# Performance work log

Measured on AMD Instinct MI355X. Metric: run time of the kernel, lower is better.

Reference implementation:

```python
import jax, jax.numpy as jnp
import numpy as np

B, N, C, H = 4, 1024, 1024, 16
DH = C // H  # 64
EPS = 1e-5   # nn.LayerNorm default


def _layernorm(x, g, b):
    m = x.mean(-1, keepdims=True)
    v = ((x - m) ** 2).mean(-1, keepdims=True)
    return (x - m) * jax.lax.rsqrt(v + EPS) * g + b


def _rot_half(x):
    d = x.shape[-1] // 2
    return jnp.concatenate([-x[..., d:], x[..., :d]], axis=-1)


def _apply_rope_cat(x, emb):
    # emb: [N, 2*DH] = sin || cos (torch tensor_split(2, -1) order)
    sin, cos = jnp.split(emb, 2, axis=-1)  # each [N, DH]
    return x * cos + _rot_half(x) * sin


def setup_inputs() -> dict:
    key = jax.random.key(0)
    ks = jax.random.split(key, 12)
    s = 0.02
    x = jax.random.normal(ks[0], (B, N, C), jnp.float32)
    delta_t_emb = jax.random.normal(ks[1], (B, N, C), jnp.float32)
    v_residual_v1 = jax.random.normal(ks[2], (B, H, N, DH), jnp.float32)
    # realistic rope table: sin||cos, each DH wide (freqs repeated twice for rotate_half)
    pos = jnp.arange(N, dtype=jnp.float32)
    inv_freq = 1.0 / (10000.0 ** (jnp.arange(0, DH // 2, dtype=jnp.float32) / (DH // 2)))
    freqs = pos[:, None] * inv_freq[None, :]          # [N, DH/2]
    freqs = jnp.concatenate([freqs, freqs], axis=-1)  # [N, DH]
    rope = jnp.concatenate([jnp.sin(freqs), jnp.cos(freqs)], axis=-1)  # [N, 2*DH]
    Wqkv = jax.random.normal(ks[3], (3 * C, C), jnp.float32) * s
    bqkv = jnp.zeros((3 * C,), jnp.float32)
    Wdt = jax.random.normal(ks[4], (3 * C, C), jnp.float32) * s
    bdt = jnp.zeros((3 * C,), jnp.float32)
    qn_g = jnp.ones((DH,), jnp.float32); qn_b = jnp.zeros((DH,), jnp.float32)
    kn_g = jnp.ones((DH,), jnp.float32); kn_b = jnp.zeros((DH,), jnp.float32)
    lamb1 = jnp.asarray(0.5, jnp.float32)
    lamb2 = jnp.asarray(0.5, jnp.float32)
    Wproj = jax.random.normal(ks[5], (C, C), jnp.float32) * s
    bproj = jnp.zeros((C,), jnp.float32)
    return {
        "x": x, "rope": rope, "delta_t_emb": delta_t_emb, "v_residual_v1": v_residual_v1,
        "Wqkv": Wqkv, "bqkv": bqkv, "Wdt": Wdt, "bdt": bdt,
        "qn_g": qn_g, "qn_b": qn_b, "kn_g": kn_g, "kn_b": kn_b,
        "lamb1": lamb1, "lamb2": lamb2, "Wproj": Wproj, "bproj": bproj,
    }


def reference(x, rope, delta_t_emb, v_residual_v1, Wqkv, bqkv, Wdt, bdt,
              qn_g, qn_b, kn_g, kn_b, lamb1, lamb2, Wproj, bproj):
    b, n, c = x.shape
    # fused QKV: [B,N,3C] -> [3,B,H,N,DH]
    qkv = (jnp.einsum('bnc,oc->bno', x, Wqkv) + bqkv).reshape(b, n, 3, H, DH)
    qkv = jnp.transpose(qkv, (2, 0, 3, 1, 4))
    q, k, v = qkv[0], qkv[1], qkv[2]
    # delta-t additive embeddings
    dqkv = (jnp.einsum('bnc,oc->bno', delta_t_emb, Wdt) + bdt).reshape(b, n, 3, H, DH)
    dqkv = jnp.transpose(dqkv, (2, 0, 3, 1, 4))
    q = q + dqkv[0]; k = k + dqkv[1]; v = v + dqkv[2]
    # value-residual mixing
    v = lamb1 * v + lamb2 * v_residual_v1
    # qk layernorm over head_dim
    q = _layernorm(q, qn_g, qn_b)
    k = _layernorm(k, kn_g, kn_b)
    # RoPE (num_prefix_tokens = 0, rotate_half=True)
    q = _apply_rope_cat(q, rope)
    k = _apply_rope_cat(k, rope)
    # SDPA, non-causal, no dropout
    scale = 1.0 / jnp.sqrt(jnp.asarray(DH, x.dtype))
    scores = jnp.einsum('bhqd,bhkd->bhqk', q, k) * scale
    attn = jax.nn.softmax(scores, axis=-1)
    out = jnp.einsum('bhqk,bhkd->bhqd', attn, v)
    # [B,H,N,DH] -> [B,N,C], output norm is Identity (scale_norm=False)
    out = jnp.transpose(out, (0, 2, 1, 3)).reshape(b, n, c)
    out = jnp.einsum('bnc,oc->bno', out, Wproj) + bproj
    return out
```

## Files before the change

kernel.cpp:

```cpp
#include <hip/hip_runtime.h>
#include <stdint.h>

typedef unsigned short u16;
typedef __attribute__((ext_vector_type(8))) short short8;
typedef __attribute__((ext_vector_type(4))) float f32x4;
typedef __attribute__((ext_vector_type(4))) unsigned short u16x4;
typedef __attribute__((ext_vector_type(4))) unsigned int u32x4;

#define DEVI __device__ __forceinline__

DEVI u16 f2bf(float f) {
  uint32_t u = __builtin_bit_cast(uint32_t, f);
  u += 0x7fffu + ((u >> 16) & 1u);
  return (u16)(u >> 16);
}

DEVI float bf2f(u16 u) {
  uint32_t v = ((uint32_t)u) << 16;
  return __builtin_bit_cast(float, v);
}

DEVI uint32_t cvt_pk_bf16(float lo, float hi) {
  uint32_t r;
  asm("v_cvt_pk_bf16_f32 %0, %1, %2" : "=v"(r) : "v"(lo), "v"(hi));
  return r;
}

DEVI void gload_lds16(const void* g, void* l) {
  __builtin_amdgcn_global_load_lds(
      (const __attribute__((address_space(1))) void*)g,
      (__attribute__((address_space(3))) void*)(uint32_t)(uintptr_t)l,
      16, 0, 0);
}

__global__ void cvt_all(const float* __restrict__ x, const float* __restrict__ dte,
                        const float* __restrict__ Wqkv, const float* __restrict__ Wdt,
                        const float* __restrict__ Wproj,
                        u16* __restrict__ A_cat, u16* __restrict__ W_cat,
                        u16* __restrict__ Wp) {
  const long T0 = (long)4096 * 2048 / 4;
  const long T1 = (long)3072 * 2048 / 4;
  const long T2 = (long)1024 * 1024 / 4;
  for (long v = (long)blockIdx.x * 256 + threadIdx.x; v < T0 + T1 + T2;
       v += (long)gridDim.x * 256) {
    const float* src;
    u16* dst;
    if (v < T0) {
      const long i = v * 4;
      const long row = i >> 11, c = i & 2047;
      src = (c < 1024) ? (x + row * 1024 + c) : (dte + row * 1024 + (c - 1024));
      dst = A_cat + i;
    } else if (v < T0 + T1) {
      const long i = (v - T0) * 4;
      const long row = i >> 11, c = i & 2047;
      src = (c < 1024) ? (Wqkv + row * 1024 + c) : (Wdt + row * 1024 + (c - 1024));
      dst = W_cat + i;
    } else {
      const long i = (v - T0 - T1) * 4;
      src = Wproj + i;
      dst = Wp + i;
    }
    const float4 f = *(const float4*)src;
    u16x4 o = {f2bf(f.x), f2bf(f.y), f2bf(f.z), f2bf(f.w)};
    *(u16x4*)dst = o;
  }
}

__global__ __launch_bounds__(256, 2)
void gemm_bt64(const u16* __restrict__ A, const u16* __restrict__ B,
               float* __restrict__ C, const float* __restrict__ bias1,
               int M, int N, int K) {
  __shared__ u16 As[64 * 32];
  __shared__ u16 Bs[128 * 32];
  const int t = threadIdx.x;
  const int w = t >> 6, l = t & 63;
  const int l15 = l & 15, lg = l >> 4;
  const int bm = blockIdx.x, bn = blockIdx.y;
  const int wr = (w >> 1) * 32, wc = (w & 1) * 64;
  f32x4 acc[2][4] = {};
  const int su = (l & 7) ^ (l >> 3);
  const int rsub = 2 * (l >> 3) + (su >> 2);
  const int sg = su & 3;
  const int sfr = (lg + 4 * (l15 & 1)) ^ (l15 >> 1);
  const int lh = l15 >> 1;

  for (int kt = 0; kt < (K >> 5); ++kt) {
    {
      const int r = w * 16 + rsub;
      gload_lds16(A + (long)(bm * 64 + r) * K + kt * 32 + sg * 8,
                  (char*)As + (w * 8) * 128);
    }
#pragma unroll
    for (int i = 0; i < 2; ++i) {
      const int r = i * 64 + w * 16 + rsub;
      gload_lds16(B + (long)(bn * 128 + r) * K + kt * 32 + sg * 8,
                  (char*)Bs + (i * 32 + w * 8) * 128);
    }
    __syncthreads();
    short8 af[2], bfr[4];
#pragma unroll
    for (int m = 0; m < 2; ++m)
      af[m] = *(const short8*)&As[((w >> 1) * 16 + m * 8 + lh) * 64 + sfr * 8];
#pragma unroll
    for (int n = 0; n < 4; ++n)
      bfr[n] = *(const short8*)&Bs[((w & 1) * 32 + n * 8 + lh) * 64 + sfr * 8];
#pragma unroll
    for (int m = 0; m < 2; ++m)
#pragma unroll
      for (int n = 0; n < 4; ++n)
        acc[m][n] = __builtin_amdgcn_mfma_f32_16x16x32_bf16(af[m], bfr[n], acc[m][n], 0, 0, 0);
    __syncthreads();
  }
#pragma unroll
  for (int m = 0; m < 2; ++m) {
    const int row0 = bm * 64 + wr + m * 16 + lg * 4;
#pragma unroll
    for (int n = 0; n < 4; ++n) {
      const int col = bn * 128 + wc + n * 16 + l15;
      const float bia = bias1 ? bias1[col] : 0.f;
#pragma unroll
      for (int r = 0; r < 4; ++r)
        C[(long)(row0 + r) * N + col] = acc[m][n][r] + bia;
    }
  }
}

__global__ __launch_bounds__(256, 2)
void gemm_bt_b16(const u16* __restrict__ A, const u16* __restrict__ B,
                 u16* __restrict__ C, const float* __restrict__ bias1,
                 const float* __restrict__ bias2, int M, int N, int K) {
  __shared__ u16 As[128 * 32];
  __shared__ u16 Bs[128 * 32];
  const int t = threadIdx.x;
  const int w = t >> 6, l = t & 63;
  const int l15 = l & 15, lg = l >> 4;
  const int bm = blockIdx.x, bn = blockIdx.y;
  const int wr = (w >> 1) * 64, wc = (w & 1) * 64;
  const int wrh = (w >> 1) * 32, wch = (w & 1) * 32;
  f32x4 acc[4][4] = {};
  const int su = (l & 7) ^ (l >> 3);
  const int rsub = 2 * (l >> 3) + (su >> 2);
  const int sg = su & 3;
  const int sfr = (lg + 4 * (l15 & 1)) ^ (l15 >> 1);
  const int lh = l15 >> 1;

  for (int kt = 0; kt < (K >> 5); ++kt) {
#pragma unroll
    for (int i = 0; i < 2; ++i) {
      const int r = i * 64 + w * 16 + rsub;
      gload_lds16(A + (long)(bm * 128 + r) * K + kt * 32 + sg * 8,
                  (char*)As + (i * 32 + w * 8) * 128);
      gload_lds16(B + (long)(bn * 128 + r) * K + kt * 32 + sg * 8,
                  (char*)Bs + (i * 32 + w * 8) * 128);
    }
    __syncthreads();
    short8 af[4], bfr[4];
#pragma unroll
    for (int m = 0; m < 4; ++m)
      af[m] = *(const short8*)&As[(wrh + m * 8 + lh) * 64 + sfr * 8];
#pragma unroll
    for (int n = 0; n < 4; ++n)
      bfr[n] = *(const short8*)&Bs[(wch + n * 8 + lh) * 64 + sfr * 8];
#pragma unroll
    for (int m = 0; m < 4; ++m)
#pragma unroll
      for (int n = 0; n < 4; ++n)
        acc[m][n] = __builtin_amdgcn_mfma_f32_16x16x32_bf16(af[m], bfr[n], acc[m][n], 0, 0, 0);
    __syncthreads();
  }
#pragma unroll
  for (int m = 0; m < 4; ++m) {
    const int row0 = bm * 128 + wr + m * 16 + lg * 4;
#pragma unroll
    for (int n = 0; n < 4; ++n) {
      const int col = bn * 128 + wc + n * 16 + l15;
      float bia = 0.f;
      if (bias1) bia += bias1[col];
      if (bias2) bia += bias2[col];
#pragma unroll
      for (int r = 0; r < 4; ++r)
        C[(long)(row0 + r) * N + col] = f2bf(acc[m][n][r] + bia);
    }
  }
}

__global__ __launch_bounds__(256)
void fuse_qkv2(const u16* __restrict__ qkv, const float* __restrict__ vres,
               const float* __restrict__ rope,
               const float* __restrict__ qg, const float* __restrict__ qb,
               const float* __restrict__ kg, const float* __restrict__ kb,
               const float* __restrict__ pl1, const float* __restrict__ pl2,
               u16* __restrict__ Q, u16* __restrict__ Ksw, u16* __restrict__ VTsw) {
  __shared__ u16 Vl[64][72];
  const int t = threadIdx.x, w = t >> 6, d = t & 63;
  const int bh = blockIdx.x, ntile = blockIdx.y;
  const int b = bh >> 4, h = bh & 15, n0 = ntile * 64;
  const float l1 = pl1[0], l2 = pl2[0];
  const float gq = qg[d], bq = qb[d];
  const float gk = kg[d], bk = kb[d];
  const float sgn = (d < 32) ? -1.f : 1.f;
  const int c = d >> 3, d7 = d & 7;

  for (int i = 0; i < 16; ++i) {
    const int nl = w * 16 + i;
    const int n = n0 + nl;
    const long base = ((long)(b * 1024 + n)) * 3072 + h * 64 + d;
    float q = bf2f(qkv[base]);
    float k = bf2f(qkv[base + 1024]);
    float v = bf2f(qkv[base + 2048]);
    v = l1 * v + l2 * vres[((long)(bh * 1024 + n)) * 64 + d];
    const float sinv = rope[n * 128 + d];
    const float cosv = rope[n * 128 + 64 + d];
    float s = q;
#pragma unroll
    for (int off = 1; off < 64; off <<= 1) s += __shfl_xor(s, off);
    const float qc = q - s * (1.f / 64.f);
    float vs = qc * qc;
#pragma unroll
    for (int off = 1; off < 64; off <<= 1) vs += __shfl_xor(vs, off);
    const float qn = qc * (1.f / sqrtf(vs * (1.f / 64.f) + 1e-5f)) * gq + bq;
    float s2 = k;
#pragma unroll
    for (int off = 1; off < 64; off <<= 1) s2 += __shfl_xor(s2, off);
    const float kc = k - s2 * (1.f / 64.f);
    float vs2 = kc * kc;
#pragma unroll
    for (int off = 1; off < 64; off <<= 1) vs2 += __shfl_xor(vs2, off);
    const float kn = kc * (1.f / sqrtf(vs2 * (1.f / 64.f) + 1e-5f)) * gk + bk;
    const float qo = __shfl_xor(qn, 32);
    const float ko = __shfl_xor(kn, 32);
    const float qr = qn * cosv + sgn * qo * sinv;
    const float kr = kn * cosv + sgn * ko * sinv;
    Q[(long)bh * 65536 + (long)n * 64 + d] = f2bf(qr);
    Ksw[(long)bh * 65536 + (long)n * 64 + ((c ^ (n & 7)) * 8 + d7)] = f2bf(kr);
    Vl[nl][d] = f2bf(v);
  }
  __syncthreads();
#pragma unroll
  for (int i = 0; i < 2; ++i) {
    const int task = i * 256 + t;
    const int dd = task >> 3, cc = task & 7;
    short8 o;
#pragma unroll
    for (int u = 0; u < 8; ++u) o[u] = (short)Vl[cc * 8 + u][dd];
    *(short8*)&VTsw[((long)(bh * 64 + dd)) * 1024 + n0 + ((cc ^ (dd & 7)) * 8)] = o;
  }
}

__global__ __launch_bounds__(256, 4)
void attn_fwd8(const u16* __restrict__ Q, const u16* __restrict__ Ksw,
               const u16* __restrict__ VTsw, u16* __restrict__ Out) {
  __shared__ u16 Kl[128 * 64];
  __shared__ u16 Vl[64 * 128];
  const int t = threadIdx.x, w = t >> 6, l = t & 63;
  const int l15 = l & 15, lg = l >> 4;
  const int x7 = l15 & 7;
  const int bh = blockIdx.x, q0 = blockIdx.y * 64;
  const long bo = (long)bh * 65536;
  const bool hihalf = (l & 16) != 0;

  const int qrow = q0 + w * 16 + l15;
  short8 qf[2];
#pragma unroll
  for (int ks = 0; ks < 2; ++ks)
    qf[ks] = *(const short8*)&Q[bo + (long)qrow * 64 + ks * 32 + lg * 8];

  f32x4 acc[4] = {};
  float m_run = -1e30f, l_run = 0.f;

  for (int kb = 0; kb < 8; ++kb) {
    const int kvb = kb * 128;
#pragma unroll
    for (int i = 0; i < 4; ++i) {
      const int idx = i * 256 + t;
      const int krow = idx >> 3, kseg = idx & 7;
      gload_lds16(Ksw + bo + (long)(kvb + krow) * 64 + kseg * 8, (char*)Kl + idx * 16);
      const int vd = idx >> 4, vc = idx & 15;
      gload_lds16(VTsw + bo + (long)vd * 1024 + kvb + vc * 8,
                  (char*)Vl + vd * 256 + vc * 16);
    }
    __syncthreads();
#pragma unroll
    for (int tb = 0; tb < 2; ++tb) {
      f32x4 p[4];
#pragma unroll
      for (int mt = 0; mt < 4; ++mt) {
        f32x4 ps = {};
#pragma unroll
        for (int ks = 0; ks < 2; ++ks) {
          const short8 kf = *(const short8*)&Kl[(tb * 64 + mt * 16 + l15) * 64 +
                                                (((ks * 4 + lg) ^ x7) * 8)];
          ps = __builtin_amdgcn_mfma_f32_16x16x32_bf16(kf, qf[ks], ps, 0, 0, 0);
        }
        p[mt] = ps;
      }
      float mx = p[0][0];
#pragma unroll
      for (int mt = 0; mt < 4; ++mt)
#pragma unroll
        for (int r = 0; r < 4; ++r) mx = fmaxf(mx, p[mt][r]);
      mx = fmaxf(mx, __shfl_xor(mx, 16));
      mx = fmaxf(mx, __shfl_xor(mx, 32));
      const float mnew = fmaxf(m_run, mx * 0.125f);
      const float alpha = __expf(m_run - mnew);
      m_run = mnew;
      float sum = 0.f;
#pragma unroll
      for (int mt = 0; mt < 4; ++mt)
#pragma unroll
        for (int r = 0; r < 4; ++r) {
          const float e = __expf(p[mt][r] * 0.125f - mnew);
          p[mt][r] = e;
          sum += e;
        }
      sum += __shfl_xor(sum, 16);
      sum += __shfl_xor(sum, 32);
      l_run = l_run * alpha + sum;
      uint32_t u0[4], u1[4];
#pragma unroll
      for (int mt = 0; mt < 4; ++mt) {
        u0[mt] = cvt_pk_bf16(p[mt][0], p[mt][1]);
        u1[mt] = cvt_pk_bf16(p[mt][2], p[mt][3]);
      }
#pragma unroll
      for (int mt = 0; mt < 4; ++mt)
#pragma unroll
        for (int r = 0; r < 4; ++r) acc[mt][r] *= alpha;
#pragma unroll
      for (int ks = 0; ks < 2; ++ks) {
        uint32_t X0 = u0[2 * ks], Y0 = u0[2 * ks + 1];
        asm("v_permlane32_swap_b32 %0, %1" : "+v"(X0), "+v"(Y0));
        uint32_t X1 = u1[2 * ks], Y1 = u1[2 * ks + 1];
        asm("v_permlane32_swap_b32 %0, %1" : "+v"(X1), "+v"(Y1));
        const uint32_t Xs0 = (uint32_t)__shfl_xor((int)X0, 16);
        const uint32_t Ys0 = (uint32_t)__shfl_xor((int)Y0, 16);
        const uint32_t Xs1 = (uint32_t)__shfl_xor((int)X1, 16);
        const uint32_t Ys1 = (uint32_t)__shfl_xor((int)Y1, 16);
        u32x4 pv;
        pv[0] = hihalf ? Ys0 : X0;
        pv[1] = hihalf ? Ys1 : X1;
        pv[2] = hihalf ? Y0 : Xs0;
        pv[3] = hihalf ? Y1 : Xs1;
        const short8 pf = __builtin_bit_cast(short8, pv);
#pragma unroll
        for (int mt = 0; mt < 4; ++mt) {
          const short8 vf = *(const short8*)&Vl[(mt * 16 + l15) * 128 + tb * 64 +
                                                (((ks * 4 + lg) ^ x7) * 8)];
          acc[mt] = __builtin_amdgcn_mfma_f32_16x16x32_bf16(vf, pf, acc[mt], 0, 0, 0);
        }
      }
    }
    __syncthreads();
  }
  const int b = bh >> 4, h = bh & 15;
  const float inv = 1.f / l_run;
  const long obase = ((long)(b * 1024 + qrow)) * 1024 + h * 64;
#pragma unroll
  for (int mt = 0; mt < 4; ++mt) {
    const long o = obase + mt * 16 + lg * 4;
    *(uint32_t*)&Out[o] = cvt_pk_bf16(acc[mt][0] * inv, acc[mt][1] * inv);
    *(uint32_t*)&Out[o + 2] = cvt_pk_bf16(acc[mt][2] * inv, acc[mt][3] * inv);
  }
}

extern "C" void kernel_launch(void* const* d_in, const int* in_sizes, int n_in,
                              void* d_out, int out_size, void* d_ws, size_t ws_size,
                              hipStream_t stream) {
  const float* x     = (const float*)d_in[0];
  const float* rope  = (const float*)d_in[1];
  const float* dte   = (const float*)d_in[2];
  const float* vres  = (const float*)d_in[3];
  const float* Wqkv  = (const float*)d_in[4];
  const float* bqkv  = (const float*)d_in[5];
  const float* Wdt   = (const float*)d_in[6];
  const float* bdt   = (const float*)d_in[7];
  const float* qn_g  = (const float*)d_in[8];
  const float* qn_b  = (const float*)d_in[9];
  const float* kn_g  = (const float*)d_in[10];
  const float* kn_b  = (const float*)d_in[11];
  const float* l1    = (const float*)d_in[12];
  const float* l2    = (const float*)d_in[13];
  const float* Wproj = (const float*)d_in[14];
  const float* bproj = (const float*)d_in[15];
  float* out = (float*)d_out;

  char* ws = (char*)d_ws;
  u16*   A_cat = (u16*)(ws);
  u16*   W_cat = (u16*)(ws + 16777216);
  u16*   Wp    = (u16*)(ws + 29360128);
  u16*   qkvb  = (u16*)(ws + 31457280);
  u16*   Qb    = (u16*)(ws + 56623104);
  u16*   Ksw   = (u16*)(ws + 65011712);
  u16*   VTsw  = (u16*)(ws + 73400320);
  u16*   AO    = (u16*)(ws + 81788928);

  cvt_all<<<2048, 256, 0, stream>>>(x, dte, Wqkv, Wdt, Wproj, A_cat, W_cat, Wp);
  gemm_bt_b16<<<dim3(32, 24), 256, 0, stream>>>(A_cat, W_cat, qkvb, bqkv, bdt,
                                                4096, 3072, 2048);
  fuse_qkv2<<<dim3(64, 16), 256, 0, stream>>>(qkvb, vres, rope, qn_g, qn_b, kn_g, kn_b,
                                              l1, l2, Qb, Ksw, VTsw);
  attn_fwd8<<<dim3(64, 16), 256, 0, stream>>>(Qb, Ksw, VTsw, AO);
  gemm_bt64<<<dim3(64, 8), 256, 0, stream>>>(AO, Wp, out, bproj, 4096, 1024, 1024);
}
```

Measured before the change: 161.4 us.

## Fuse QK layernorm, RoPE, value-residual mix and V transpose into QKV GEMM epilogue

Moves the per-head layernorm, RoPE, value-residual mixing and swizzled Q/K/VT writes into the epilogue of the QKV GEMM. This drops the intermediate bf16 qkv buffer and the separate fuse_qkv2 launch. The epilogue reduces over 16-lane shuffles per token row and stages V through an extra LDS buffer with two-phase synchronisation. The added LDS and register pressure could lower GEMM occupancy, and the Q/K stores are scattered 2-byte writes.

```diff
diff --git a/kernel.cpp b/kernel.cpp
--- a/kernel.cpp
+++ b/kernel.cpp
@@ -126,11 +126,17 @@
 }
 
 __global__ __launch_bounds__(256, 2)
-void gemm_bt_b16(const u16* __restrict__ A, const u16* __restrict__ B,
-                 u16* __restrict__ C, const float* __restrict__ bias1,
-                 const float* __restrict__ bias2, int M, int N, int K) {
+void gemm_qkv_fused(const u16* __restrict__ A, const u16* __restrict__ B,
+                    const float* __restrict__ bqkv, const float* __restrict__ bdt,
+                    const float* __restrict__ vres, const float* __restrict__ rope,
+                    const float* __restrict__ qg, const float* __restrict__ qb,
+                    const float* __restrict__ kg, const float* __restrict__ kb,
+                    const float* __restrict__ pl1, const float* __restrict__ pl2,
+                    u16* __restrict__ Q, u16* __restrict__ Ksw,
+                    u16* __restrict__ VTsw, int M, int N, int K) {
   __shared__ u16 As[128 * 32];
   __shared__ u16 Bs[128 * 32];
+  __shared__ u16 vsc[2][64][66];
   const int t = threadIdx.x;
   const int w = t >> 6, l = t & 63;
   const int l15 = l & 15, lg = l >> 4;
@@ -168,82 +174,106 @@
         acc[m][n] = __builtin_amdgcn_mfma_f32_16x16x32_bf16(af[m], bfr[n], acc[m][n], 0, 0, 0);
     __syncthreads();
   }
-#pragma unroll
-  for (int m = 0; m < 4; ++m) {
-    const int row0 = bm * 128 + wr + m * 16 + lg * 4;
+
+  float biasv[4];
+#pragma unroll
+  for (int n = 0; n < 4; ++n) {
+    const int col = bn * 128 + wc + n * 16 + l15;
+    biasv[n] = bqkv[col] + bdt[col];
+  }
+  const int h = (bn & 7) * 2 + (wc >> 6);
+
+  if (bn < 16) {
+    const bool isQ = (bn < 8);
+    const float* gp = isQ ? qg : kg;
+    const float* bp = isQ ? qb : kb;
+    float gv[4], bvv[4];
 #pragma unroll
     for (int n = 0; n < 4; ++n) {
-      const int col = bn * 128 + wc + n * 16 + l15;
-      float bia = 0.f;
-      if (bias1) bia += bias1[col];
-      if (bias2) bia += bias2[col];
-#pragma unroll
-      for (int r = 0; r < 4; ++r)
-        C[(long)(row0 + r) * N + col] = f2bf(acc[m][n][r] + bia);
-    }
-  }
-}
-
-__global__ __launch_bounds__(256)
-void fuse_qkv2(const u16* __restrict__ qkv, const float* __restrict__ vres,
-               const float* __restrict__ rope,
-               const float* __restrict__ qg, const float* __restrict__ qb,
-               const float* __restrict__ kg, const float* __restrict__ kb,
-               const float* __restrict__ pl1, const float* __restrict__ pl2,
-               u16* __restrict__ Q, u16* __restrict__ Ksw, u16* __restrict__ VTsw) {
-  __shared__ u16 Vl[64][72];
-  const int t = threadIdx.x, w = t >> 6, d = t & 63;
-  const int bh = blockIdx.x, ntile = blockIdx.y;
-  const int b = bh >> 4, h = bh & 15, n0 = ntile * 64;
-  const float l1 = pl1[0], l2 = pl2[0];
-  const float gq = qg[d], bq = qb[d];
-  const float gk = kg[d], bk = kb[d];
-  const float sgn = (d < 32) ? -1.f : 1.f;
-  const int c = d >> 3, d7 = d & 7;
-
-  for (int i = 0; i < 16; ++i) {
-    const int nl = w * 16 + i;
-    const int n = n0 + nl;
-    const long base = ((long)(b * 1024 + n)) * 3072 + h * 64 + d;
-    float q = bf2f(qkv[base]);
-    float k = bf2f(qkv[base + 1024]);
-    float v = bf2f(qkv[base + 2048]);
-    v = l1 * v + l2 * vres[((long)(bh * 1024 + n)) * 64 + d];
-    const float sinv = rope[n * 128 + d];
-    const float cosv = rope[n * 128 + 64 + d];
-    float s = q;
-#pragma unroll
-    for (int off = 1; off < 64; off <<= 1) s += __shfl_xor(s, off);
-    const float qc = q - s * (1.f / 64.f);
-    float vs = qc * qc;
-#pragma unroll
-    for (int off = 1; off < 64; off <<= 1) vs += __shfl_xor(vs, off);
-    const float qn = qc * (1.f / sqrtf(vs * (1.f / 64.f) + 1e-5f)) * gq + bq;
-    float s2 = k;
-#pragma unroll
-    for (int off = 1; off < 64; off <<= 1) s2 += __shfl_xor(s2, off);
-    const float kc = k - s2 * (1.f / 64.f);
-    float vs2 = kc * kc;
-#pragma unroll
-    for (int off = 1; off < 64; off <<= 1) vs2 += __shfl_xor(vs2, off);
-    const float kn = kc * (1.f / sqrtf(vs2 * (1.f / 64.f) + 1e-5f)) * gk + bk;
-    const float qo = __shfl_xor(qn, 32);
-    const float ko = __shfl_xor(kn, 32);
-    const float qr = qn * cosv + sgn * qo * sinv;
-    const float kr = kn * cosv + sgn * ko * sinv;
-    Q[(long)bh * 65536 + (long)n * 64 + d] = f2bf(qr);
-    Ksw[(long)bh * 65536 + (long)n * 64 + ((c ^ (n & 7)) * 8 + d7)] = f2bf(kr);
-    Vl[nl][d] = f2bf(v);
-  }
-  __syncthreads();
-#pragma unroll
-  for (int i = 0; i < 2; ++i) {
-    const int task = i * 256 + t;
-    const int dd = task >> 3, cc = task & 7;
-    short8 o;
-#pragma unroll
-    for (int u = 0; u < 8; ++u) o[u] = (short)Vl[cc * 8 + u][dd];
-    *(short8*)&VTsw[((long)(bh * 64 + dd)) * 1024 + n0 + ((cc ^ (dd & 7)) * 8)] = o;
+      gv[n] = gp[n * 16 + l15];
+      bvv[n] = bp[n * 16 + l15];
+    }
+#pragma unroll
+    for (int m = 0; m < 4; ++m) {
+#pragma unroll
+      for (int r = 0; r < 4; ++r) {
+        const int tok = bm * 128 + wr + m * 16 + lg * 4 + r;
+        const int ntk = tok & 1023, bb = tok >> 10;
+        float vals[4];
+#pragma unroll
+        for (int n = 0; n < 4; ++n) vals[n] = acc[m][n][r] + biasv[n];
+        float s = vals[0] + vals[1] + vals[2] + vals[3];
+#pragma unroll
+        for (int off = 1; off < 16; off <<= 1) s += __shfl_xor(s, off);
+        const float mean = s * (1.f / 64.f);
+        float cn[4], vs = 0.f;
+#pragma unroll
+        for (int n = 0; n < 4; ++n) {
+          cn[n] = vals[n] - mean;
+          vs += cn[n] * cn[n];
+        }
+#pragma unroll
+        for (int off = 1; off < 16; off <<= 1) vs += __shfl_xor(vs, off);
+        const float rstd = 1.f / sqrtf(vs * (1.f / 64.f) + 1e-5f);
+        float norm[4];
+#pragma unroll
+        for (int n = 0; n < 4; ++n) norm[n] = cn[n] * rstd * gv[n] + bvv[n];
+        const long rb = (long)ntk * 128;
+        const long obase = (long)(bb * 16 + h) * 65536 + (long)ntk * 64;
+#pragma unroll
+        for (int n = 0; n < 4; ++n) {
+          const float sinv = rope[rb + n * 16 + l15];
+          const float cosv = rope[rb + 64 + n * 16 + l15];
+          const float sgn = (n < 2) ? -1.f : 1.f;
+          const float outv = norm[n] * cosv + sgn * norm[n ^ 2] * sinv;
+          if (isQ) {
+            Q[obase + n * 16 + l15] = f2bf(outv);
+          } else {
+            const int c = n * 2 + (l15 >> 3);
+            Ksw[obase + ((c ^ (ntk & 7)) * 8) + (l15 & 7)] = f2bf(outv);
+          }
+        }
+      }
+    }
+  } else {
+    const float l1 = pl1[0], l2 = pl2[0];
+    const int hv = (bn - 16) * 2 + (wc >> 6);
+    const int myphase = w >> 1, widx = w & 1;
+    const int tokbase = bm * 128 + wr;
+    const int ntk0 = tokbase & 1023, bbw = tokbase >> 10;
+    const long vrb = ((long)(bbw * 16 + hv) * 1024 + ntk0) * 64;
+    const long vtb = (long)(bbw * 16 + hv) * 64;
+#pragma unroll
+    for (int p = 0; p < 2; ++p) {
+      if (myphase == p) {
+#pragma unroll
+        for (int m = 0; m < 4; ++m)
+#pragma unroll
+          for (int r = 0; r < 4; ++r) {
+            const int tl = m * 16 + lg * 4 + r;
+#pragma unroll
+            for (int n = 0; n < 4; ++n) {
+              const int d = n * 16 + l15;
+              const float vv = l1 * (acc[m][n][r] + biasv[n]) +
+                               l2 * vres[vrb + (long)tl * 64 + d];
+              vsc[widx][tl][d] = f2bf(vv);
+            }
+          }
+      }
+      __syncthreads();
+      if (myphase == p) {
+#pragma unroll
+        for (int it = 0; it < 8; ++it) {
+          const int task = it * 64 + l;
+          const int dd = task >> 3, cc = task & 7;
+          short8 o;
+#pragma unroll
+          for (int u = 0; u < 8; ++u) o[u] = (short)vsc[widx][cc * 8 + u][dd];
+          *(short8*)&VTsw[(vtb + dd) * 1024 + ntk0 + ((cc ^ (dd & 7)) * 8)] = o;
+        }
+      }
+      __syncthreads();
+    }
   }
 }
 
@@ -388,17 +418,15 @@
   u16*   A_cat = (u16*)(ws);
   u16*   W_cat = (u16*)(ws + 16777216);
   u16*   Wp    = (u16*)(ws + 29360128);
-  u16*   qkvb  = (u16*)(ws + 31457280);
   u16*   Qb    = (u16*)(ws + 56623104);
   u16*   Ksw   = (u16*)(ws + 65011712);
   u16*   VTsw  = (u16*)(ws + 73400320);
   u16*   AO    = (u16*)(ws + 81788928);
 
   cvt_all<<<2048, 256, 0, stream>>>(x, dte, Wqkv, Wdt, Wproj, A_cat, W_cat, Wp);
-  gemm_bt_b16<<<dim3(32, 24), 256, 0, stream>>>(A_cat, W_cat, qkvb, bqkv, bdt,
-                                                4096, 3072, 2048);
-  fuse_qkv2<<<dim3(64, 16), 256, 0, stream>>>(qkvb, vres, rope, qn_g, qn_b, kn_g, kn_b,
-                                              l1, l2, Qb, Ksw, VTsw);
+  gemm_qkv_fused<<<dim3(32, 24), 256, 0, stream>>>(
+      A_cat, W_cat, bqkv, bdt, vres, rope, qn_g, qn_b, kn_g, kn_b, l1, l2,
+      Qb, Ksw, VTsw, 4096, 3072, 2048);
   attn_fwd8<<<dim3(64, 16), 256, 0, stream>>>(Qb, Ksw, VTsw, AO);
   gemm_bt64<<<dim3(64, 8), 256, 0, stream>>>(AO, Wp, out, bproj, 4096, 1024, 1024);
 }
```

New measurement: 146.7 us. 9.1% less time.

## Write QKV GEMM output head-major and vectorize LayerNorm/RoPE fuse kernel

Applied to the files above, without the earlier changes.

The QKV GEMM epilogue now scatters its results straight into separate head-major Q, K and V raw buffers instead of one interleaved [B,N,3C] buffer. The fuse kernel is rewritten so that each token row is handled by 4 lanes with 16-byte vector loads and stores. That row-per-4-lanes mapping turns the 64-wide shuffle reductions into 2-step shuffles and cuts per-element scalar loads. The GEMM stores become more scattered, and the bias pointers are now assumed to be non-null.

```diff
diff --git a/kernel.cpp b/kernel.cpp
--- a/kernel.cpp
+++ b/kernel.cpp
@@ -126,9 +126,10 @@
 }
 
 __global__ __launch_bounds__(256, 2)
-void gemm_bt_b16(const u16* __restrict__ A, const u16* __restrict__ B,
-                 u16* __restrict__ C, const float* __restrict__ bias1,
-                 const float* __restrict__ bias2, int M, int N, int K) {
+void gemm_qkv_hm(const u16* __restrict__ A, const u16* __restrict__ B,
+                 const float* __restrict__ bias1, const float* __restrict__ bias2,
+                 u16* __restrict__ Qraw, u16* __restrict__ Kraw,
+                 u16* __restrict__ Vraw, int M, int N, int K) {
   __shared__ u16 As[128 * 32];
   __shared__ u16 Bs[128 * 32];
   const int t = threadIdx.x;
@@ -168,72 +169,165 @@
         acc[m][n] = __builtin_amdgcn_mfma_f32_16x16x32_bf16(af[m], bfr[n], acc[m][n], 0, 0, 0);
     __syncthreads();
   }
+  u16* Traw = (bn < 8) ? Qraw : (bn < 16) ? Kraw : Vraw;
+  const int h = ((bn & 7) << 1) | (wc >> 6);
+  const long tb = ((long)((bm >> 3) * 16 + h)) << 16;
+  const int nnbase = (bm & 7) * 128 + wr;
 #pragma unroll
   for (int m = 0; m < 4; ++m) {
-    const int row0 = bm * 128 + wr + m * 16 + lg * 4;
 #pragma unroll
     for (int n = 0; n < 4; ++n) {
       const int col = bn * 128 + wc + n * 16 + l15;
-      float bia = 0.f;
-      if (bias1) bia += bias1[col];
-      if (bias2) bia += bias2[col];
-#pragma unroll
-      for (int r = 0; r < 4; ++r)
-        C[(long)(row0 + r) * N + col] = f2bf(acc[m][n][r] + bia);
+      float bia = bias1[col] + bias2[col];
+      const int d = n * 16 + l15;
+#pragma unroll
+      for (int r = 0; r < 4; ++r) {
+        const int nn = nnbase + m * 16 + lg * 4 + r;
+        Traw[tb + (long)nn * 64 + d] = f2bf(acc[m][n][r] + bia);
+      }
     }
   }
 }
 
 __global__ __launch_bounds__(256)
-void fuse_qkv2(const u16* __restrict__ qkv, const float* __restrict__ vres,
+void fuse_qkv4(const u16* __restrict__ Qraw, const u16* __restrict__ Kraw,
+               const u16* __restrict__ Vraw, const float* __restrict__ vres,
                const float* __restrict__ rope,
                const float* __restrict__ qg, const float* __restrict__ qb,
                const float* __restrict__ kg, const float* __restrict__ kb,
                const float* __restrict__ pl1, const float* __restrict__ pl2,
                u16* __restrict__ Q, u16* __restrict__ Ksw, u16* __restrict__ VTsw) {
   __shared__ u16 Vl[64][72];
-  const int t = threadIdx.x, w = t >> 6, d = t & 63;
+  const int t = threadIdx.x, w = t >> 6, l = t & 63;
+  const int c4 = l & 3;
+  const int tg = l >> 2;
+  const int d0 = c4 * 8;
   const int bh = blockIdx.x, ntile = blockIdx.y;
-  const int b = bh >> 4, h = bh & 15, n0 = ntile * 64;
-  const float l1 = pl1[0], l2 = pl2[0];
-  const float gq = qg[d], bq = qb[d];
-  const float gk = kg[d], bk = kb[d];
-  const float sgn = (d < 32) ? -1.f : 1.f;
-  const int c = d >> 3, d7 = d & 7;
-
-  for (int i = 0; i < 16; ++i) {
-    const int nl = w * 16 + i;
-    const int n = n0 + nl;
-    const long base = ((long)(b * 1024 + n)) * 3072 + h * 64 + d;
-    float q = bf2f(qkv[base]);
-    float k = bf2f(qkv[base + 1024]);
-    float v = bf2f(qkv[base + 2048]);
-    v = l1 * v + l2 * vres[((long)(bh * 1024 + n)) * 64 + d];
-    const float sinv = rope[n * 128 + d];
-    const float cosv = rope[n * 128 + 64 + d];
-    float s = q;
-#pragma unroll
-    for (int off = 1; off < 64; off <<= 1) s += __shfl_xor(s, off);
-    const float qc = q - s * (1.f / 64.f);
-    float vs = qc * qc;
-#pragma unroll
-    for (int off = 1; off < 64; off <<= 1) vs += __shfl_xor(vs, off);
-    const float qn = qc * (1.f / sqrtf(vs * (1.f / 64.f) + 1e-5f)) * gq + bq;
-    float s2 = k;
-#pragma unroll
-    for (int off = 1; off < 64; off <<= 1) s2 += __shfl_xor(s2, off);
-    const float kc = k - s2 * (1.f / 64.f);
-    float vs2 = kc * kc;
-#pragma unroll
-    for (int off = 1; off < 64; off <<= 1) vs2 += __shfl_xor(vs2, off);
-    const float kn = kc * (1.f / sqrtf(vs2 * (1.f / 64.f) + 1e-5f)) * gk + bk;
-    const float qo = __shfl_xor(qn, 32);
-    const float ko = __shfl_xor(kn, 32);
-    const float qr = qn * cosv + sgn * qo * sinv;
-    const float kr = kn * cosv + sgn * ko * sinv;
-    Q[(long)bh * 65536 + (long)n * 64 + d] = f2bf(qr);
-    Ksw[(long)bh * 65536 + (long)n * 64 + ((c ^ (n & 7)) * 8 + d7)] = f2bf(kr);
-    Vl[nl][d] = f2bf(v);
+  const int n0 = ntile * 64;
+  const int tl = w * 16 + tg;
+  const int n = n0 + tl;
+  const long obase = (long)bh * 65536 + (long)n * 64;
+  const int nx = n & 7;
+
+  float sn_lo[8], sn_hi[8], cs_lo[8], cs_hi[8];
+  {
+    const float4 a0 = *(const float4*)&rope[n * 128 + d0];
+    const float4 a1 = *(const float4*)&rope[n * 128 + d0 + 4];
+    const float4 b0 = *(const float4*)&rope[n * 128 + 32 + d0];
+    const float4 b1 = *(const float4*)&rope[n * 128 + 32 + d0 + 4];
+    const float4 c0 = *(const float4*)&rope[n * 128 + 64 + d0];
+    const float4 c1 = *(const float4*)&rope[n * 128 + 64 + d0 + 4];
+    const float4 e0 = *(const float4*)&rope[n * 128 + 96 + d0];
+    const float4 e1 = *(const float4*)&rope[n * 128 + 96 + d0 + 4];
+    sn_lo[0]=a0.x; sn_lo[1]=a0.y; sn_lo[2]=a0.z; sn_lo[3]=a0.w;
+    sn_lo[4]=a1.x; sn_lo[5]=a1.y; sn_lo[6]=a1.z; sn_lo[7]=a1.w;
+    sn_hi[0]=b0.x; sn_hi[1]=b0.y; sn_hi[2]=b0.z; sn_hi[3]=b0.w;
+    sn_hi[4]=b1.x; sn_hi[5]=b1.y; sn_hi[6]=b1.z; sn_hi[7]=b1.w;
+    cs_lo[0]=c0.x; cs_lo[1]=c0.y; cs_lo[2]=c0.z; cs_lo[3]=c0.w;
+    cs_lo[4]=c1.x; cs_lo[5]=c1.y; cs_lo[6]=c1.z; cs_lo[7]=c1.w;
+    cs_hi[0]=e0.x; cs_hi[1]=e0.y; cs_hi[2]=e0.z; cs_hi[3]=e0.w;
+    cs_hi[4]=e1.x; cs_hi[5]=e1.y; cs_hi[6]=e1.z; cs_hi[7]=e1.w;
+  }
+
+  {
+    const short8 xlo = *(const short8*)&Qraw[obase + d0];
+    const short8 xhi = *(const short8*)&Qraw[obase + 32 + d0];
+    float vlo[8], vhi[8];
+    float s = 0.f;
+#pragma unroll
+    for (int u = 0; u < 8; ++u) {
+      vlo[u] = bf2f((u16)xlo[u]);
+      vhi[u] = bf2f((u16)xhi[u]);
+      s += vlo[u] + vhi[u];
+    }
+    s += __shfl_xor(s, 1); s += __shfl_xor(s, 2);
+    const float mean = s * (1.f / 64.f);
+    float vs = 0.f;
+#pragma unroll
+    for (int u = 0; u < 8; ++u) {
+      vlo[u] -= mean; vhi[u] -= mean;
+      vs += vlo[u] * vlo[u] + vhi[u] * vhi[u];
+    }
+    vs += __shfl_xor(vs, 1); vs += __shfl_xor(vs, 2);
+    const float rstd = 1.f / sqrtf(vs * (1.f / 64.f) + 1e-5f);
+    float olo[8], ohi[8];
+#pragma unroll
+    for (int u = 0; u < 8; ++u) {
+      const float nl_ = vlo[u] * rstd * qg[d0 + u] + qb[d0 + u];
+      const float nh_ = vhi[u] * rstd * qg[32 + d0 + u] + qb[32 + d0 + u];
+      olo[u] = nl_ * cs_lo[u] - nh_ * sn_lo[u];
+      ohi[u] = nh_ * cs_hi[u] + nl_ * sn_hi[u];
+    }
+    u32x4 plo, phi;
+#pragma unroll
+    for (int u = 0; u < 4; ++u) {
+      plo[u] = cvt_pk_bf16(olo[2 * u], olo[2 * u + 1]);
+      phi[u] = cvt_pk_bf16(ohi[2 * u], ohi[2 * u + 1]);
+    }
+    *(u32x4*)&Q[obase + d0] = plo;
+    *(u32x4*)&Q[obase + 32 + d0] = phi;
+  }
+
+  {
+    const short8 xlo = *(const short8*)&Kraw[obase + d0];
+    const short8 xhi = *(const short8*)&Kraw[obase + 32 + d0];
+    float vlo[8], vhi[8];
+    float s = 0.f;
+#pragma unroll
+    for (int u = 0; u < 8; ++u) {
+      vlo[u] = bf2f((u16)xlo[u]);
+      vhi[u] = bf2f((u16)xhi[u]);
+      s += vlo[u] + vhi[u];
+    }
+    s += __shfl_xor(s, 1); s += __shfl_xor(s, 2);
+    const float mean = s * (1.f / 64.f);
+    float vs = 0.f;
+#pragma unroll
+    for (int u = 0; u < 8; ++u) {
+      vlo[u] -= mean; vhi[u] -= mean;
+      vs += vlo[u] * vlo[u] + vhi[u] * vhi[u];
+    }
+    vs += __shfl_xor(vs, 1); vs += __shfl_xor(vs, 2);
+    const float rstd = 1.f / sqrtf(vs * (1.f / 64.f) + 1e-5f);
+    float olo[8], ohi[8];
+#pragma unroll
+    for (int u = 0; u < 8; ++u) {
+      const float nl_ = vlo[u] * rstd * kg[d0 + u] + kb[d0 + u];
+      const float nh_ = vhi[u] * rstd * kg[32 + d0 + u] + kb[32 + d0 + u];
+      olo[u] = nl_ * cs_lo[u] - nh_ * sn_lo[u];
+      ohi[u] = nh_ * cs_hi[u] + nl_ * sn_hi[u];
+    }
+    u32x4 plo, phi;
+#pragma unroll
+    for (int u = 0; u < 4; ++u) {
+      plo[u] = cvt_pk_bf16(olo[2 * u], olo[2 * u + 1]);
+      phi[u] = cvt_pk_bf16(ohi[2 * u], ohi[2 * u + 1]);
+    }
+    *(u32x4*)&Ksw[obase + ((c4 ^ nx) * 8)] = plo;
+    *(u32x4*)&Ksw[obase + (((c4 + 4) ^ nx) * 8)] = phi;
+  }
+
+  {
+    const float l1 = pl1[0], l2 = pl2[0];
+    const short8 xlo = *(const short8*)&Vraw[obase + d0];
+    const short8 xhi = *(const short8*)&Vraw[obase + 32 + d0];
+    const long vb = ((long)(bh * 1024 + n)) * 64;
+    const float4 r0 = *(const float4*)&vres[vb + d0];
+    const float4 r1 = *(const float4*)&vres[vb + d0 + 4];
+    const float4 r2 = *(const float4*)&vres[vb + 32 + d0];
+    const float4 r3 = *(const float4*)&vres[vb + 32 + d0 + 4];
+    const float rl[8] = {r0.x, r0.y, r0.z, r0.w, r1.x, r1.y, r1.z, r1.w};
+    const float rh[8] = {r2.x, r2.y, r2.z, r2.w, r3.x, r3.y, r3.z, r3.w};
+    u32x4 plo, phi;
+#pragma unroll
+    for (int u = 0; u < 4; ++u) {
+      plo[u] = cvt_pk_bf16(l1 * bf2f((u16)xlo[2 * u]) + l2 * rl[2 * u],
+                           l1 * bf2f((u16)xlo[2 * u + 1]) + l2 * rl[2 * u + 1]);
+      phi[u] = cvt_pk_bf16(l1 * bf2f((u16)xhi[2 * u]) + l2 * rh[2 * u],
+                           l1 * bf2f((u16)xhi[2 * u + 1]) + l2 * rh[2 * u + 1]);
+    }
+    *(u32x4*)&Vl[tl][d0] = plo;
+    *(u32x4*)&Vl[tl][32 + d0] = phi;
   }
   __syncthreads();
 #pragma unroll
@@ -388,17 +482,20 @@
   u16*   A_cat = (u16*)(ws);
   u16*   W_cat = (u16*)(ws + 16777216);
   u16*   Wp    = (u16*)(ws + 29360128);
-  u16*   qkvb  = (u16*)(ws + 31457280);
+  u16*   Qraw  = (u16*)(ws + 31457280);
+  u16*   Kraw  = (u16*)(ws + 39845888);
+  u16*   Vraw  = (u16*)(ws + 48234496);
   u16*   Qb    = (u16*)(ws + 56623104);
   u16*   Ksw   = (u16*)(ws + 65011712);
   u16*   VTsw  = (u16*)(ws + 73400320);
   u16*   AO    = (u16*)(ws + 81788928);
 
   cvt_all<<<2048, 256, 0, stream>>>(x, dte, Wqkv, Wdt, Wproj, A_cat, W_cat, Wp);
-  gemm_bt_b16<<<dim3(32, 24), 256, 0, stream>>>(A_cat, W_cat, qkvb, bqkv, bdt,
-                                                4096, 3072, 2048);
-  fuse_qkv2<<<dim3(64, 16), 256, 0, stream>>>(qkvb, vres, rope, qn_g, qn_b, kn_g, kn_b,
-                                              l1, l2, Qb, Ksw, VTsw);
+  gemm_qkv_hm<<<dim3(32, 24), 256, 0, stream>>>(A_cat, W_cat, bqkv, bdt,
+                                                Qraw, Kraw, Vraw, 4096, 3072, 2048);
+  fuse_qkv4<<<dim3(64, 16), 256, 0, stream>>>(Qraw, Kraw, Vraw, vres, rope,
+                                              qn_g, qn_b, kn_g, kn_b, l1, l2,
+                                              Qb, Ksw, VTsw);
   attn_fwd8<<<dim3(64, 16), 256, 0, stream>>>(Qb, Ksw, VTsw, AO);
   gemm_bt64<<<dim3(64, 8), 256, 0, stream>>>(AO, Wp, out, bproj, 4096, 1024, 1024);
 }
```

After: 146.2 us. 9.4% less time.

## Write QKV GEMM output head-major and split LN/RoPE and V fuse kernels

Applied to the files above, without the earlier changes.

The QKV GEMM epilogue now scatters results directly into separate head-major Q, K, V raw buffers instead of one interleaved [B,N,3C] buffer. The post-processing is split into a Q/K layernorm+RoPE kernel that uses 16-byte vector loads with only a 4-lane shuffle reduction, and a V kernel that does the residual mix plus transpose through LDS with vectorized reads. The goal is to replace the strided scalar loads and 64-wide shuffle reductions of the old fused kernel. In exchange there is one extra kernel launch, and the GEMM epilogue stores may be less coalesced.

```diff
diff --git a/kernel.cpp b/kernel.cpp
--- a/kernel.cpp
+++ b/kernel.cpp
@@ -126,16 +126,17 @@
 }
 
 __global__ __launch_bounds__(256, 2)
-void gemm_bt_b16(const u16* __restrict__ A, const u16* __restrict__ B,
-                 u16* __restrict__ C, const float* __restrict__ bias1,
-                 const float* __restrict__ bias2, int M, int N, int K) {
+void gemm_qkv_hm(const u16* __restrict__ A, const u16* __restrict__ B,
+                 const float* __restrict__ bias1, const float* __restrict__ bias2,
+                 u16* __restrict__ Qraw, u16* __restrict__ Kraw,
+                 u16* __restrict__ Vraw, int M, int N, int K) {
   __shared__ u16 As[128 * 32];
   __shared__ u16 Bs[128 * 32];
   const int t = threadIdx.x;
   const int w = t >> 6, l = t & 63;
   const int l15 = l & 15, lg = l >> 4;
   const int bm = blockIdx.x, bn = blockIdx.y;
-  const int wr = (w >> 1) * 64, wc = (w & 1) * 64;
+  const int wc = (w & 1) * 64;
   const int wrh = (w >> 1) * 32, wch = (w & 1) * 32;
   f32x4 acc[4][4] = {};
   const int su = (l & 7) ^ (l >> 3);
@@ -168,82 +169,137 @@
         acc[m][n] = __builtin_amdgcn_mfma_f32_16x16x32_bf16(af[m], bfr[n], acc[m][n], 0, 0, 0);
     __syncthreads();
   }
+  u16* Traw = (bn < 8) ? Qraw : (bn < 16) ? Kraw : Vraw;
+  const int h = ((bn & 7) << 1) | (wc >> 6);
+  const long tb = ((long)((bm >> 3) * 16 + h)) << 16;
+  const int nnbase = (bm & 7) * 128 + (w >> 1) * 64;
 #pragma unroll
   for (int m = 0; m < 4; ++m) {
-    const int row0 = bm * 128 + wr + m * 16 + lg * 4;
 #pragma unroll
     for (int n = 0; n < 4; ++n) {
       const int col = bn * 128 + wc + n * 16 + l15;
-      float bia = 0.f;
-      if (bias1) bia += bias1[col];
-      if (bias2) bia += bias2[col];
-#pragma unroll
-      for (int r = 0; r < 4; ++r)
-        C[(long)(row0 + r) * N + col] = f2bf(acc[m][n][r] + bia);
+      float bia = bias1[col] + bias2[col];
+      const int d = n * 16 + l15;
+#pragma unroll
+      for (int r = 0; r < 4; ++r) {
+        const int nn = nnbase + m * 16 + lg * 4 + r;
+        Traw[tb + (long)nn * 64 + d] = f2bf(acc[m][n][r] + bia);
+      }
     }
   }
 }
 
 __global__ __launch_bounds__(256)
-void fuse_qkv2(const u16* __restrict__ qkv, const float* __restrict__ vres,
-               const float* __restrict__ rope,
-               const float* __restrict__ qg, const float* __restrict__ qb,
-               const float* __restrict__ kg, const float* __restrict__ kb,
-               const float* __restrict__ pl1, const float* __restrict__ pl2,
-               u16* __restrict__ Q, u16* __restrict__ Ksw, u16* __restrict__ VTsw) {
-  __shared__ u16 Vl[64][72];
-  const int t = threadIdx.x, w = t >> 6, d = t & 63;
+void fuse_qk(const u16* __restrict__ Qraw, const u16* __restrict__ Kraw,
+             const float* __restrict__ rope,
+             const float* __restrict__ qg, const float* __restrict__ qb,
+             const float* __restrict__ kg, const float* __restrict__ kb,
+             u16* __restrict__ Q, u16* __restrict__ Ksw) {
+  const int t = threadIdx.x, w = t >> 6, l = t & 63;
+  const int c4 = l & 3;
+  const int tg = l >> 2;
+  const int d0 = c4 * 8;
   const int bh = blockIdx.x, ntile = blockIdx.y;
-  const int b = bh >> 4, h = bh & 15, n0 = ntile * 64;
+  const int n = ntile * 64 + w * 16 + tg;
+  const long obase = (long)bh * 65536 + (long)n * 64;
+  const int nx = n & 7;
+
+#define LNROPE_PHASE(SRC, GP, BP, STORE_LO, STORE_HI)                          \
+  {                                                                            \
+    const short8 xlo = *(const short8*)&SRC[obase + d0];                       \
+    const short8 xhi = *(const short8*)&SRC[obase + 32 + d0];                  \
+    float vlo[8], vhi[8];                                                      \
+    float s = 0.f;                                                             \
+    _Pragma("unroll") for (int u = 0; u < 8; ++u) {                            \
+      vlo[u] = bf2f((u16)xlo[u]);                                              \
+      vhi[u] = bf2f((u16)xhi[u]);                                              \
+      s += vlo[u] + vhi[u];                                                    \
+    }                                                                          \
+    s += __shfl_xor(s, 1); s += __shfl_xor(s, 2);                              \
+    const float mean = s * (1.f / 64.f);                                       \
+    float vs = 0.f;                                                            \
+    _Pragma("unroll") for (int u = 0; u < 8; ++u) {                            \
+      vlo[u] -= mean; vhi[u] -= mean;                                          \
+      vs += vlo[u] * vlo[u] + vhi[u] * vhi[u];                                 \
+    }                                                                          \
+    vs += __shfl_xor(vs, 1); vs += __shfl_xor(vs, 2);                          \
+    const float rstd = 1.f / sqrtf(vs * (1.f / 64.f) + 1e-5f);                 \
+    u32x4 plo, phi;                                                            \
+    _Pragma("unroll") for (int p2 = 0; p2 < 2; ++p2) {                         \
+      const int db = p2 * 4;                                                   \
+      const float4 gl = *(const float4*)&GP[d0 + db];                          \
+      const float4 bl = *(const float4*)&BP[d0 + db];                          \
+      const float4 gh = *(const float4*)&GP[32 + d0 + db];                     \
+      const float4 bhh = *(const float4*)&BP[32 + d0 + db];                    \
+      const float4 snl = *(const float4*)&rope[n * 128 + d0 + db];             \
+      const float4 snh = *(const float4*)&rope[n * 128 + 32 + d0 + db];        \
+      const float4 csl = *(const float4*)&rope[n * 128 + 64 + d0 + db];        \
+      const float4 csh = *(const float4*)&rope[n * 128 + 96 + d0 + db];        \
+      float ol[4], oh[4];                                                      \
+      _Pragma("unroll") for (int u = 0; u < 4; ++u) {                          \
+        const float gl_u = ((const float*)&gl)[u], bl_u = ((const float*)&bl)[u]; \
+        const float gh_u = ((const float*)&gh)[u], bh_u = ((const float*)&bhh)[u]; \
+        const float nl_ = vlo[db + u] * rstd * gl_u + bl_u;                    \
+        const float nh_ = vhi[db + u] * rstd * gh_u + bh_u;                    \
+        ol[u] = nl_ * ((const float*)&csl)[u] - nh_ * ((const float*)&snl)[u]; \
+        oh[u] = nh_ * ((const float*)&csh)[u] + nl_ * ((const float*)&snh)[u]; \
+      }                                                                        \
+      plo[p2 * 2] = cvt_pk_bf16(ol[0], ol[1]);                                 \
+      plo[p2 * 2 + 1] = cvt_pk_bf16(ol[2], ol[3]);                             \
+      phi[p2 * 2] = cvt_pk_bf16(oh[0], oh[1]);                                 \
+      phi[p2 * 2 + 1] = cvt_pk_bf16(oh[2], oh[3]);                             \
+    }                                                                          \
+    *(u32x4*)&STORE_LO = plo;                                                  \
+    *(u32x4*)&STORE_HI = phi;                                                  \
+  }
+
+  LNROPE_PHASE(Qraw, qg, qb, Q[obase + d0], Q[obase + 32 + d0])
+  LNROPE_PHASE(Kraw, kg, kb, Ksw[obase + ((c4 ^ nx) * 8)],
+               Ksw[obase + (((c4 + 4) ^ nx) * 8)])
+#undef LNROPE_PHASE
+}
+
+__global__ __launch_bounds__(256)
+void fuse_v(const u16* __restrict__ Vraw, const float* __restrict__ vres,
+            const float* __restrict__ pl1, const float* __restrict__ pl2,
+            u16* __restrict__ VTsw) {
+  __shared__ u16 VlT[64][70];
+  const int t = threadIdx.x, w = t >> 6, l = t & 63;
+  const int c4 = l & 3;
+  const int tg = l >> 2;
+  const int d0 = c4 * 8;
+  const int bh = blockIdx.x, ntile = blockIdx.y;
+  const int n0 = ntile * 64;
+  const int tl = w * 16 + tg;
+  const int n = n0 + tl;
+  const long obase = (long)bh * 65536 + (long)n * 64;
   const float l1 = pl1[0], l2 = pl2[0];
-  const float gq = qg[d], bq = qb[d];
-  const float gk = kg[d], bk = kb[d];
-  const float sgn = (d < 32) ? -1.f : 1.f;
-  const int c = d >> 3, d7 = d & 7;
-
-  for (int i = 0; i < 16; ++i) {
-    const int nl = w * 16 + i;
-    const int n = n0 + nl;
-    const long base = ((long)(b * 1024 + n)) * 3072 + h * 64 + d;
-    float q = bf2f(qkv[base]);
-    float k = bf2f(qkv[base + 1024]);
-    float v = bf2f(qkv[base + 2048]);
-    v = l1 * v + l2 * vres[((long)(bh * 1024 + n)) * 64 + d];
-    const float sinv = rope[n * 128 + d];
-    const float cosv = rope[n * 128 + 64 + d];
-    float s = q;
-#pragma unroll
-    for (int off = 1; off < 64; off <<= 1) s += __shfl_xor(s, off);
-    const float qc = q - s * (1.f / 64.f);
-    float vs = qc * qc;
-#pragma unroll
-    for (int off = 1; off < 64; off <<= 1) vs += __shfl_xor(vs, off);
-    const float qn = qc * (1.f / sqrtf(vs * (1.f / 64.f) + 1e-5f)) * gq + bq;
-    float s2 = k;
-#pragma unroll
-    for (int off = 1; off < 64; off <<= 1) s2 += __shfl_xor(s2, off);
-    const float kc = k - s2 * (1.f / 64.f);
-    float vs2 = kc * kc;
-#pragma unroll
-    for (int off = 1; off < 64; off <<= 1) vs2 += __shfl_xor(vs2, off);
-    const float kn = kc * (1.f / sqrtf(vs2 * (1.f / 64.f) + 1e-5f)) * gk + bk;
-    const float qo = __shfl_xor(qn, 32);
-    const float ko = __shfl_xor(kn, 32);
-    const float qr = qn * cosv + sgn * qo * sinv;
-    const float kr = kn * cosv + sgn * ko * sinv;
-    Q[(long)bh * 65536 + (long)n * 64 + d] = f2bf(qr);
-    Ksw[(long)bh * 65536 + (long)n * 64 + ((c ^ (n & 7)) * 8 + d7)] = f2bf(kr);
-    Vl[nl][d] = f2bf(v);
+
+  {
+    const short8 xlo = *(const short8*)&Vraw[obase + d0];
+    const short8 xhi = *(const short8*)&Vraw[obase + 32 + d0];
+    const long vb = ((long)(bh * 1024 + n)) * 64;
+    const float4 r0 = *(const float4*)&vres[vb + d0];
+    const float4 r1 = *(const float4*)&vres[vb + d0 + 4];
+    const float4 r2 = *(const float4*)&vres[vb + 32 + d0];
+    const float4 r3 = *(const float4*)&vres[vb + 32 + d0 + 4];
+    const float rl[8] = {r0.x, r0.y, r0.z, r0.w, r1.x, r1.y, r1.z, r1.w};
+    const float rh[8] = {r2.x, r2.y, r2.z, r2.w, r3.x, r3.y, r3.z, r3.w};
+#pragma unroll
+    for (int u = 0; u < 8; ++u) {
+      VlT[d0 + u][tl] = f2bf(l1 * bf2f((u16)xlo[u]) + l2 * rl[u]);
+      VlT[32 + d0 + u][tl] = f2bf(l1 * bf2f((u16)xhi[u]) + l2 * rh[u]);
+    }
   }
   __syncthreads();
+  const uint32_t* base = (const uint32_t*)&VlT[0][0];
 #pragma unroll
   for (int i = 0; i < 2; ++i) {
     const int task = i * 256 + t;
     const int dd = task >> 3, cc = task & 7;
-    short8 o;
-#pragma unroll
-    for (int u = 0; u < 8; ++u) o[u] = (short)Vl[cc * 8 + u][dd];
-    *(short8*)&VTsw[((long)(bh * 64 + dd)) * 1024 + n0 + ((cc ^ (dd & 7)) * 8)] = o;
+    const uint32_t* p = base + dd * 35 + cc * 4;
+    u32x4 o = {p[0], p[1], p[2], p[3]};
+    *(u32x4*)&VTsw[((long)(bh * 64 + dd)) * 1024 + n0 + ((cc ^ (dd & 7)) * 8)] = o;
   }
 }
 
@@ -388,17 +444,20 @@
   u16*   A_cat = (u16*)(ws);
   u16*   W_cat = (u16*)(ws + 16777216);
   u16*   Wp    = (u16*)(ws + 29360128);
-  u16*   qkvb  = (u16*)(ws + 31457280);
+  u16*   Qraw  = (u16*)(ws + 31457280);
+  u16*   Kraw  = (u16*)(ws + 39845888);
+  u16*   Vraw  = (u16*)(ws + 48234496);
   u16*   Qb    = (u16*)(ws + 56623104);
   u16*   Ksw   = (u16*)(ws + 65011712);
   u16*   VTsw  = (u16*)(ws + 73400320);
   u16*   AO    = (u16*)(ws + 81788928);
 
   cvt_all<<<2048, 256, 0, stream>>>(x, dte, Wqkv, Wdt, Wproj, A_cat, W_cat, Wp);
-  gemm_bt_b16<<<dim3(32, 24), 256, 0, stream>>>(A_cat, W_cat, qkvb, bqkv, bdt,
-                                                4096, 3072, 2048);
-  fuse_qkv2<<<dim3(64, 16), 256, 0, stream>>>(qkvb, vres, rope, qn_g, qn_b, kn_g, kn_b,
-                                              l1, l2, Qb, Ksw, VTsw);
+  gemm_qkv_hm<<<dim3(32, 24), 256, 0, stream>>>(A_cat, W_cat, bqkv, bdt,
+                                                Qraw, Kraw, Vraw, 4096, 3072, 2048);
+  fuse_qk<<<dim3(64, 16), 256, 0, stream>>>(Qraw, Kraw, rope, qn_g, qn_b,
+                                            kn_g, kn_b, Qb, Ksw);
+  fuse_v<<<dim3(64, 16), 256, 0, stream>>>(Vraw, vres, l1, l2, VTsw);
   attn_fwd8<<<dim3(64, 16), 256, 0, stream>>>(Qb, Ksw, VTsw, AO);
   gemm_bt64<<<dim3(64, 8), 256, 0, stream>>>(AO, Wp, out, bproj, 4096, 1024, 1024);
 }
```

Result: faster. 149.9 us (-7.1%).
